# Optimization experiments

Hardware: AMD Instinct MI355X
Metric: run time of the kernel (lower is better)

## Reference

```python
import jax, jax.numpy as jnp
import numpy as np

TOPK = 4


def setup_inputs() -> dict:
    key = jax.random.key(0)
    ks = jax.random.split(key, 9)
    B, T, D = 4, 2048, 1024
    E, H = 32, 128          # routed experts, per-expert hidden
    HS = H * TOPK           # shared expert hidden = 512
    s = lambda k, shape, fan: jax.random.normal(k, shape, dtype=jnp.float32) / np.sqrt(fan)
    return {
        "x": jax.random.normal(ks[0], (B, T, D), dtype=jnp.float32),
        "router_w": s(ks[1], (E, D), D),
        "router_bias": jnp.zeros((E,), dtype=jnp.float32),
        "gate_w": s(ks[2], (E, H, D), D),
        "up_w": s(ks[3], (E, H, D), D),
        "down_w": s(ks[4], (E, D, H), H),
        "sgate_w": s(ks[5], (HS, D), D),
        "sup_w": s(ks[6], (HS, D), D),
        "sdown_w": s(ks[7], (D, HS), HS),
    }


def reference(x, router_w, router_bias, gate_w, up_w, down_w, sgate_w, sup_w, sdown_w):
    B, T, D = x.shape
    flat = x.reshape(B * T, D)                                   # [N, D]
    # Router (fp32 logits + persistent bias buffer)
    logits = flat.astype(jnp.float32) @ router_w.T + router_bias  # [N, E]
    scores = jax.nn.softmax(logits, axis=-1)
    topk_scores, topk_idx = jax.lax.top_k(scores, TOPK)          # [N, K]
    topk_scores = topk_scores / jnp.clip(
        topk_scores.sum(axis=-1, keepdims=True), 1e-12, None)
    # Dense all-expert SwiGLU (matches torch.stack over experts)
    h = jax.nn.silu(jnp.einsum("nd,ehd->neh", flat, gate_w)) \
        * jnp.einsum("nd,ehd->neh", flat, up_w)                  # [N, E, H]
    expert_out = jnp.einsum("neh,edh->ned", h, down_w)           # [N, E, D]
    # Gather top-k expert outputs, scale, combine
    sel = jnp.take_along_axis(expert_out, topk_idx[:, :, None], axis=1)  # [N, K, D]
    out = (sel * topk_scores.astype(flat.dtype)[:, :, None]).sum(axis=1)  # [N, D]
    # Always-on shared expert (SwiGLU)
    out = out + (jax.nn.silu(flat @ sgate_w.T) * (flat @ sup_w.T)) @ sdown_w.T
    return out.reshape(B, T, D)
```

## Files before the change

kernel.cpp:

```cpp
#include <hip/hip_runtime.h>
#include <hip/hip_bf16.h>
#include <math.h>

#define N_TOK 8192
#define DIM   1024
#define E_R   32
#define H_E   128
#define HS    512
#define TOPK  4
#define RKS   8
#define RKL   (DIM / RKS)
#define MAXSLOT 34816

typedef __bf16 bf16;
typedef __bf16 bf16x8 __attribute__((ext_vector_type(8)));
typedef float  floatx4 __attribute__((ext_vector_type(4)));

#define MFMA16(a,b,c) __builtin_amdgcn_mfma_f32_16x16x32_bf16(a,b,c,0,0,0)

__device__ __forceinline__ void gl_lds16(const bf16* g, bf16* l) {
    __builtin_amdgcn_global_load_lds(
        (const __attribute__((address_space(1))) void*)g,
        (__attribute__((address_space(3))) void*)l, 16, 0, 0);
}

__global__ __launch_bounds__(256)
void cvt_all(const float* __restrict__ x, const float* __restrict__ g,
             const float* __restrict__ u, const float* __restrict__ d,
             const float* __restrict__ sg, const float* __restrict__ su,
             const float* __restrict__ sd,
             bf16* __restrict__ xb, bf16* __restrict__ gb, bf16* __restrict__ ub,
             bf16* __restrict__ db, bf16* __restrict__ sgb, bf16* __restrict__ sub,
             bf16* __restrict__ sdb) {
    int b = blockIdx.x;
    const float* s; bf16* o; int lb;
    if      (b < 4096)  { s = x;  o = xb;  lb = b; }
    else if (b < 6144)  { s = g;  o = gb;  lb = b - 4096; }
    else if (b < 8192)  { s = u;  o = ub;  lb = b - 6144; }
    else if (b < 10240) { s = d;  o = db;  lb = b - 8192; }
    else if (b < 10496) { s = sg; o = sgb; lb = b - 10240; }
    else if (b < 10752) { s = su; o = sub; lb = b - 10496; }
    else                { s = sd; o = sdb; lb = b - 10752; }
    size_t i = (size_t)lb * 2048 + threadIdx.x * 8;
    float4 v0 = *(const float4*)(s + i);
    float4 v1 = *(const float4*)(s + i + 4);
    bf16x8 r = {(bf16)v0.x,(bf16)v0.y,(bf16)v0.z,(bf16)v0.w,
                (bf16)v1.x,(bf16)v1.y,(bf16)v1.z,(bf16)v1.w};
    *(bf16x8*)(o + i) = r;
}

__global__ __launch_bounds__(256)
void router_gemm(const float* __restrict__ x, const float* __restrict__ rw,
                 float* __restrict__ partial) {
    __shared__ float Xs[64 * 132];
    __shared__ float Wt[128 * 32];
    int tid = threadIdx.x;
    int t0  = blockIdx.x * 64;
    int kb  = blockIdx.y * RKL;

#pragma unroll
    for (int j = 0; j < 8; ++j) {
        int flat = j * 1024 + tid * 4;
        int row = flat >> 7, col = flat & 127;
        float4 v = *(const float4*)(x + (size_t)(t0 + row) * DIM + kb + col);
        *(float4*)(&Xs[row * 132 + col]) = v;
    }
    {
        int e = tid >> 3, kq = (tid & 7) * 16;
        const float* wp = rw + (size_t)e * DIM + kb + kq;
#pragma unroll
        for (int i = 0; i < 16; i += 4) {
            float4 v = *(const float4*)(wp + i);
            Wt[(kq + i + 0) * 32 + e] = v.x;
            Wt[(kq + i + 1) * 32 + e] = v.y;
            Wt[(kq + i + 2) * 32 + e] = v.z;
            Wt[(kq + i + 3) * 32 + e] = v.w;
        }
    }
    __syncthreads();

    int eg = tid & 7, tg = tid >> 3;
    float acc[2][4] = {{0.f}};
#pragma unroll 4
    for (int k = 0; k < RKL; k += 4) {
        float4 xa0 = *(const float4*)(&Xs[(tg * 2 + 0) * 132 + k]);
        float4 xa1 = *(const float4*)(&Xs[(tg * 2 + 1) * 132 + k]);
#pragma unroll
        for (int kk = 0; kk < 4; ++kk) {
            float4 w = *(const float4*)(&Wt[(k + kk) * 32 + eg * 4]);
            float x0 = (&xa0.x)[kk], x1 = (&xa1.x)[kk];
            acc[0][0] += x0 * w.x; acc[0][1] += x0 * w.y;
            acc[0][2] += x0 * w.z; acc[0][3] += x0 * w.w;
            acc[1][0] += x1 * w.x; acc[1][1] += x1 * w.y;
            acc[1][2] += x1 * w.z; acc[1][3] += x1 * w.w;
        }
    }
#pragma unroll
    for (int t = 0; t < 2; ++t) {
        floatx4 v = { acc[t][0], acc[t][1], acc[t][2], acc[t][3] };
        *(floatx4*)(&partial[((size_t)blockIdx.y * N_TOK + t0 + tg * 2 + t) * 32 + eg * 4]) = v;
    }
}

__global__ __launch_bounds__(256)
void router_fin(const float* __restrict__ partial, const float* __restrict__ rb,
                int* __restrict__ counts, int* __restrict__ tlist,
                float* __restrict__ slist, int* __restrict__ tok2slot) {
    __shared__ int lcnt[E_R];
    __shared__ int gbase[E_R];
    int tid = threadIdx.x;
    int n = blockIdx.x * 256 + tid;
    if (tid < E_R) lcnt[tid] = 0;
    __syncthreads();

    float lg[E_R];
#pragma unroll
    for (int e4 = 0; e4 < E_R; e4 += 4) {
        floatx4 s = {0.f, 0.f, 0.f, 0.f};
#pragma unroll
        for (int ks = 0; ks < RKS; ++ks)
            s += *(const floatx4*)(&partial[((size_t)ks * N_TOK + n) * 32 + e4]);
        lg[e4 + 0] = s[0] + rb[e4 + 0];
        lg[e4 + 1] = s[1] + rb[e4 + 1];
        lg[e4 + 2] = s[2] + rb[e4 + 2];
        lg[e4 + 3] = s[3] + rb[e4 + 3];
    }
    float mx = -1e30f;
#pragma unroll
    for (int e = 0; e < E_R; ++e) mx = fmaxf(mx, lg[e]);
    float se = 0.f;
#pragma unroll
    for (int e = 0; e < E_R; ++e) { float v = __expf(lg[e] - mx); lg[e] = v; se += v; }
    float inv = 1.f / se;

    unsigned usedMask = 0;
    int idx[TOPK]; float pv[TOPK]; int lpos[TOPK]; float psum = 0.f;
    for (int k = 0; k < TOPK; ++k) {
        float best = -1.f; int bi = 0;
        for (int e = 0; e < E_R; ++e)
            if (!((usedMask >> e) & 1) && lg[e] > best) { best = lg[e]; bi = e; }
        usedMask |= 1u << bi;
        idx[k] = bi; pv[k] = best * inv; psum += pv[k];
    }
    float norm = 1.f / fmaxf(psum, 1e-12f);
#pragma unroll
    for (int k = 0; k < TOPK; ++k)
        lpos[k] = atomicAdd(&lcnt[idx[k]], 1);
    __syncthreads();
    if (tid < E_R) gbase[tid] = atomicAdd(&counts[tid], lcnt[tid]);
    __syncthreads();
#pragma unroll
    for (int k = 0; k < TOPK; ++k) {
        int e = idx[k];
        int pos = gbase[e] + lpos[k];
        tlist[(size_t)e * N_TOK + pos] = n;
        slist[(size_t)e * N_TOK + pos] = pv[k] * norm;
        tok2slot[(size_t)n * 4 + k] = (e << 16) | pos;
    }
}

__global__ void wq_build(const int* __restrict__ counts, int* __restrict__ items,
                         int* __restrict__ nitems, int* __restrict__ expbase) {
    if (threadIdx.x == 0) {
        int n = 0, base = 0;
        for (int e = 0; e < E_R; ++e) {
            int c = counts[e];
            expbase[e] = base;
            int nt = (c + 63) >> 6;
            for (int t = 0; t < nt; ++t)
                items[n++] = (e << 24) | (t << 16) | (base + t * 64);
            base += nt * 64;
        }
        *nitems = n;
    }
}

__global__ __launch_bounds__(256, 4)
void phase1(const bf16* __restrict__ xb, const bf16* __restrict__ wg,
            const bf16* __restrict__ wu, const bf16* __restrict__ sg,
            const bf16* __restrict__ su, const int* __restrict__ counts,
            const int* __restrict__ tlist, const int* __restrict__ items,
            const int* __restrict__ nitems,
            bf16* __restrict__ Hg, bf16* __restrict__ Hs) {
    __shared__ __align__(16) bf16 As[2 * 64 * 32];
    __shared__ __align__(16) bf16 Bs[2 * 256 * 32];

    int b = blockIdx.x;
    const bf16 *gptr, *uptr;
    bf16* hout; int hstride;
    int e, lbase, cnt = 0;
    if (b < 512) {
        int c = b >> 7, t = b & 127;
        gptr = sg + (size_t)c * H_E * DIM;
        uptr = su + (size_t)c * H_E * DIM;
        hout = Hs + (size_t)t * 64 * HS + c * H_E;
        hstride = HS;
        lbase = t * 64;
        e = -1;
    } else {
        int rbk = b - 512;
        if (rbk >= *nitems) return;
        int it = items[rbk];
        e = it >> 24; int t = (it >> 16) & 0xff; int rowbase = it & 0xffff;
        gptr = wg + (size_t)e * H_E * DIM;
        uptr = wu + (size_t)e * H_E * DIM;
        hout = Hg + (size_t)rowbase * H_E;
        hstride = H_E;
        cnt = counts[e];
        lbase = t * 64;
    }

    int tid = threadIdx.x;
    int r = tid >> 2;
    int chunk = (((tid & 3) ^ ((tid >> 3) & 3))) * 8;
    int tok;
    if (e < 0) tok = lbase + r;
    else { int li = lbase + r; if (li >= cnt) li = cnt - 1; tok = tlist[(size_t)e * N_TOK + li]; }
    const bf16* aSrc = xb + (size_t)tok * DIM + chunk;
    const bf16* gSrc = gptr + (size_t)r * DIM + chunk;
    const bf16* uSrc = uptr + (size_t)r * DIM + chunk;

    int w = tid >> 6, lane = tid & 63, m = lane & 15, quad = lane >> 4;
    int quadx = quad ^ ((m >> 1) & 3);

    floatx4 aG[4][2] = {{{0}}};
    floatx4 aU[4][2] = {{{0}}};

    #define P1_STAGE(buf, k0)                                                  \
        do {                                                                   \
            bf16* aD = As + (buf) * 2048 + tid * 8;                            \
            bf16* bD = Bs + (buf) * 8192 + tid * 8;                            \
            gl_lds16(aSrc + (k0), aD);                                         \
            gl_lds16(gSrc + (k0), bD);                                         \
            gl_lds16(gSrc + 64 * DIM + (k0), bD + 2048);                       \
            gl_lds16(uSrc + (k0), bD + 4096);                                  \
            gl_lds16(uSrc + 64 * DIM + (k0), bD + 6144);                       \
        } while (0)

    P1_STAGE(0, 0);
    __syncthreads();

    int cur = 0;
    for (int k0 = 0; k0 < DIM; k0 += 32) {
        if (k0 + 32 < DIM) P1_STAGE(cur ^ 1, k0 + 32);
        const bf16* Ab = As + cur * 2048;
        const bf16* Bb = Bs + cur * 8192;
        bf16x8 a[4], bg[2], bu[2];
#pragma unroll
        for (int mg = 0; mg < 4; ++mg)
            a[mg] = *(const bf16x8*)(Ab + (mg * 16 + m) * 32 + quadx * 8);
#pragma unroll
        for (int j = 0; j < 2; ++j) {
            bg[j] = *(const bf16x8*)(Bb + (w * 32 + j * 16 + m) * 32 + quadx * 8);
            bu[j] = *(const bf16x8*)(Bb + (128 + w * 32 + j * 16 + m) * 32 + quadx * 8);
        }
#pragma unroll
        for (int j = 0; j < 2; ++j)
#pragma unroll
            for (int mg = 0; mg < 4; ++mg) {
                aG[mg][j] = MFMA16(a[mg], bg[j], aG[mg][j]);
                aU[mg][j] = MFMA16(a[mg], bu[j], aU[mg][j]);
            }
        __syncthreads();
        cur ^= 1;
    }
    #undef P1_STAGE

#pragma unroll
    for (int mg = 0; mg < 4; ++mg)
#pragma unroll
        for (int j = 0; j < 2; ++j)
#pragma unroll
            for (int r4 = 0; r4 < 4; ++r4) {
                float gv = aG[mg][j][r4], uv = aU[mg][j][r4];
                float h = gv / (1.f + __expf(-gv)) * uv;
                hout[(size_t)(mg * 16 + quad * 4 + r4) * hstride + w * 32 + j * 16 + m] = (bf16)h;
            }
}

__global__ __launch_bounds__(256, 4)
void phase2(const bf16* __restrict__ Hg, const bf16* __restrict__ wd,
            const int* __restrict__ counts, const float* __restrict__ slist,
            const int* __restrict__ items, const int* __restrict__ nitems,
            bf16* __restrict__ Od) {
    __shared__ __align__(16) bf16 As[2 * 64 * 32];
    __shared__ __align__(16) bf16 Bs[2 * 256 * 32];
    __shared__ float ssc[64];

    int rbk = blockIdx.x;
    if (rbk >= *nitems) return;
    int it = items[rbk];
    int e = it >> 24, t = (it >> 16) & 0xff, rowbase = it & 0xffff;
    int n0 = blockIdx.y * 256;
    int cnt = counts[e];

    int tid = threadIdx.x;
    if (tid < 64) {
        int li = t * 64 + tid;
        ssc[tid] = (li < cnt) ? slist[(size_t)e * N_TOK + li] : 0.f;
    }

    int r = tid >> 2;
    int chunk = (((tid & 3) ^ ((tid >> 3) & 3))) * 8;
    const bf16* aSrc = Hg + (size_t)(rowbase + r) * H_E + chunk;
    const bf16* bSrc = wd + (size_t)e * DIM * H_E + (size_t)(n0 + r) * H_E + chunk;

    int w = tid >> 6, lane = tid & 63, m = lane & 15, quad = lane >> 4;
    int quadx = quad ^ ((m >> 1) & 3);
    floatx4 acc[4][4] = {{{0}}};

    #define P2_STAGE(buf, k0)                                                  \
        do {                                                                   \
            bf16* aD = As + (buf) * 2048 + tid * 8;                            \
            bf16* bD = Bs + (buf) * 8192 + tid * 8;                            \
            gl_lds16(aSrc + (k0), aD);                                         \
            _Pragma("unroll")                                                  \
            for (int p = 0; p < 4; ++p)                                        \
                gl_lds16(bSrc + (size_t)p * 64 * H_E + (k0), bD + p * 2048);   \
        } while (0)

    P2_STAGE(0, 0);
    __syncthreads();

    int cur = 0;
    for (int k0 = 0; k0 < H_E; k0 += 32) {
        if (k0 + 32 < H_E) P2_STAGE(cur ^ 1, k0 + 32);
        const bf16* Ab = As + cur * 2048;
        const bf16* Bb = Bs + cur * 8192;
        bf16x8 a[4], bb[4];
#pragma unroll
        for (int mg = 0; mg < 4; ++mg)
            a[mg] = *(const bf16x8*)(Ab + (mg * 16 + m) * 32 + quadx * 8);
#pragma unroll
        for (int ng = 0; ng < 4; ++ng)
            bb[ng] = *(const bf16x8*)(Bb + (w * 64 + ng * 16 + m) * 32 + quadx * 8);
#pragma unroll
        for (int ng = 0; ng < 4; ++ng)
#pragma unroll
            for (int mg = 0; mg < 4; ++mg)
                acc[mg][ng] = MFMA16(a[mg], bb[ng], acc[mg][ng]);
        __syncthreads();
        cur ^= 1;
    }
    #undef P2_STAGE

#pragma unroll
    for (int mg = 0; mg < 4; ++mg)
#pragma unroll
        for (int r4 = 0; r4 < 4; ++r4) {
            int row = mg * 16 + quad * 4 + r4;
            float sc = ssc[row];
            bf16* op = Od + (size_t)(rowbase + row) * DIM + n0 + w * 64 + m;
#pragma unroll
            for (int ng = 0; ng < 4; ++ng)
                op[ng * 16] = (bf16)(acc[mg][ng][r4] * sc);
        }
}

__global__ __launch_bounds__(256, 4)
void shared_down(const bf16* __restrict__ Hs, const bf16* __restrict__ sd,
                 const bf16* __restrict__ Od, const int* __restrict__ tok2slot,
                 const int* __restrict__ expbase, float* __restrict__ out) {
    __shared__ __align__(16) bf16 As[2 * 64 * 32];
    __shared__ __align__(16) bf16 Bs[2 * 256 * 32];
    __shared__ int srow[64][4];

    int t0 = blockIdx.x * 64;
    int n0 = blockIdx.y * 256;
    int tid = threadIdx.x;

    if (tid < 64) {
        const int* t2s = tok2slot + (size_t)(t0 + tid) * 4;
#pragma unroll
        for (int k = 0; k < 4; ++k) {
            int v = t2s[k];
            srow[tid][k] = expbase[v >> 16] + (v & 0xffff);
        }
    }

    int r = tid >> 2;
    int chunk = (((tid & 3) ^ ((tid >> 3) & 3))) * 8;
    const bf16* aSrc = Hs + (size_t)(t0 + r) * HS + chunk;
    const bf16* bSrc = sd + (size_t)(n0 + r) * HS + chunk;

    int w = tid >> 6, lane = tid & 63, m = lane & 15, quad = lane >> 4;
    int quadx = quad ^ ((m >> 1) & 3);
    floatx4 acc[4][4] = {{{0}}};

    #define SD_STAGE(buf, k0)                                                  \
        do {                                                                   \
            bf16* aD = As + (buf) * 2048 + tid * 8;                            \
            bf16* bD = Bs + (buf) * 8192 + tid * 8;                            \
            gl_lds16(aSrc + (k0), aD);                                         \
            _Pragma("unroll")                                                  \
            for (int p = 0; p < 4; ++p)                                        \
                gl_lds16(bSrc + (size_t)p * 64 * HS + (k0), bD + p * 2048);    \
        } while (0)

    SD_STAGE(0, 0);
    __syncthreads();

    int cur = 0;
    for (int tt = 0; tt < 16; ++tt) {
        if (tt < 15) SD_STAGE(cur ^ 1, (tt + 1) * 32);
        const bf16* Ab = As + cur * 2048;
        const bf16* Bb = Bs + cur * 8192;
        bf16x8 a[4], bb[4];
#pragma unroll
        for (int mg = 0; mg < 4; ++mg)
            a[mg] = *(const bf16x8*)(Ab + (mg * 16 + m) * 32 + quadx * 8);
#pragma unroll
        for (int ng = 0; ng < 4; ++ng)
            bb[ng] = *(const bf16x8*)(Bb + (w * 64 + ng * 16 + m) * 32 + quadx * 8);
#pragma unroll
        for (int ng = 0; ng < 4; ++ng)
#pragma unroll
            for (int mg = 0; mg < 4; ++mg)
                acc[mg][ng] = MFMA16(a[mg], bb[ng], acc[mg][ng]);
        __syncthreads();
        cur ^= 1;
    }
    #undef SD_STAGE

#pragma unroll
    for (int mg = 0; mg < 4; ++mg)
#pragma unroll
        for (int r4 = 0; r4 < 4; ++r4) {
            int rl = mg * 16 + quad * 4 + r4;
            size_t r0 = (size_t)srow[rl][0] * DIM;
            size_t r1 = (size_t)srow[rl][1] * DIM;
            size_t r2 = (size_t)srow[rl][2] * DIM;
            size_t r3 = (size_t)srow[rl][3] * DIM;
            float* op = out + (size_t)(t0 + rl) * DIM + n0 + w * 64 + m;
#pragma unroll
            for (int ng = 0; ng < 4; ++ng) {
                int col = n0 + w * 64 + ng * 16 + m;
                float v = acc[mg][ng][r4]
                        + (float)Od[r0 + col] + (float)Od[r1 + col]
                        + (float)Od[r2 + col] + (float)Od[r3 + col];
                op[ng * 16] = v;
            }
        }
}

extern "C" void kernel_launch(void* const* d_in, const int* in_sizes, int n_in,
                              void* d_out, int out_size, void* d_ws, size_t ws_size,
                              hipStream_t stream) {
    (void)in_sizes; (void)n_in; (void)out_size; (void)ws_size;
    const float* x   = (const float*)d_in[0];
    const float* rw  = (const float*)d_in[1];
    const float* rb  = (const float*)d_in[2];
    const float* gw  = (const float*)d_in[3];
    const float* uw  = (const float*)d_in[4];
    const float* dw  = (const float*)d_in[5];
    const float* sgw = (const float*)d_in[6];
    const float* suw = (const float*)d_in[7];
    const float* sdw = (const float*)d_in[8];
    float* out = (float*)d_out;

    char* ws = (char*)d_ws;
    size_t o = 0;
    bf16* xb  = (bf16*)(ws + o); o += (size_t)N_TOK * DIM * 2;
    bf16* wgb = (bf16*)(ws + o); o += (size_t)E_R * H_E * DIM * 2;
    bf16* wub = (bf16*)(ws + o); o += (size_t)E_R * H_E * DIM * 2;
    bf16* wdb = (bf16*)(ws + o); o += (size_t)E_R * DIM * H_E * 2;
    bf16* sgb = (bf16*)(ws + o); o += (size_t)HS * DIM * 2;
    bf16* sub = (bf16*)(ws + o); o += (size_t)HS * DIM * 2;
    bf16* sdb = (bf16*)(ws + o); o += (size_t)DIM * HS * 2;
    bf16* Hg  = (bf16*)(ws + o); o += (size_t)MAXSLOT * H_E * 2;
    bf16* Hs  = (bf16*)(ws + o); o += (size_t)N_TOK * HS * 2;
    bf16* Od  = (bf16*)(ws + o); o += (size_t)MAXSLOT * DIM * 2;
    float* partial = (float*)(ws + o); o += (size_t)RKS * N_TOK * 32 * 4;
    int*   counts = (int*)(ws + o);   o += 256;
    int*   tlist  = (int*)(ws + o);   o += (size_t)E_R * N_TOK * 4;
    float* slist  = (float*)(ws + o); o += (size_t)E_R * N_TOK * 4;
    int*   tok2slot = (int*)(ws + o); o += (size_t)N_TOK * 4 * 4;
    int*   items  = (int*)(ws + o);   o += 4096;
    int*   nitems = (int*)(ws + o);   o += 64;
    int*   expbase = (int*)(ws + o);  o += 256;

    hipMemsetAsync(counts, 0, E_R * sizeof(int), stream);

    router_gemm<<<dim3(N_TOK / 64, RKS), 256, 0, stream>>>(x, rw, partial);
    router_fin<<<N_TOK / 256, 256, 0, stream>>>(partial, rb, counts, tlist, slist,
                                                tok2slot);
    cvt_all<<<11008, 256, 0, stream>>>(x, gw, uw, dw, sgw, suw, sdw,
                                       xb, wgb, wub, wdb, sgb, sub, sdb);
    wq_build<<<1, 64, 0, stream>>>(counts, items, nitems, expbase);
    phase1<<<1056, 256, 0, stream>>>(xb, wgb, wub, sgb, sub, counts, tlist,
                                     items, nitems, Hg, Hs);
    phase2<<<dim3(544, 4), 256, 0, stream>>>(Hg, wdb, counts, slist,
                                             items, nitems, Od);
    shared_down<<<dim3(N_TOK / 64, 4), 256, 0, stream>>>(Hs, sdb, Od, tok2slot,
                                                         expbase, out);
}
```

Baseline: 306.5 us.

## Scatter routed expert outputs into output via atomics, drop Od buffer

Phase2 now scales each routed-expert down-projection row and atomically adds it straight into the fp32 output at the token's row, using the token list. Shared_down runs first and writes the shared-expert result directly. This removes the bf16 Od intermediate (write plus four gathered reads per output element) and the tok2slot/expbase bookkeeping. In exchange phase2 issues 4 float atomics per output element, contended across the top-k experts, and summation order becomes nondeterministic.

Measured after the change: 511.2 us. 66.8% more time.

```diff
diff --git a/kernel.cpp b/kernel.cpp
--- a/kernel.cpp
+++ b/kernel.cpp
@@ -105,7 +105,7 @@
 __global__ __launch_bounds__(256)
 void router_fin(const float* __restrict__ partial, const float* __restrict__ rb,
                 int* __restrict__ counts, int* __restrict__ tlist,
-                float* __restrict__ slist, int* __restrict__ tok2slot) {
+                float* __restrict__ slist) {
     __shared__ int lcnt[E_R];
     __shared__ int gbase[E_R];
     int tid = threadIdx.x;
@@ -155,17 +155,15 @@
         int pos = gbase[e] + lpos[k];
         tlist[(size_t)e * N_TOK + pos] = n;
         slist[(size_t)e * N_TOK + pos] = pv[k] * norm;
-        tok2slot[(size_t)n * 4 + k] = (e << 16) | pos;
     }
 }
 
 __global__ void wq_build(const int* __restrict__ counts, int* __restrict__ items,
-                         int* __restrict__ nitems, int* __restrict__ expbase) {
+                         int* __restrict__ nitems) {
     if (threadIdx.x == 0) {
         int n = 0, base = 0;
         for (int e = 0; e < E_R; ++e) {
             int c = counts[e];
-            expbase[e] = base;
             int nt = (c + 63) >> 6;
             for (int t = 0; t < nt; ++t)
                 items[n++] = (e << 24) | (t << 16) | (base + t * 64);
@@ -281,11 +279,12 @@
 __global__ __launch_bounds__(256, 4)
 void phase2(const bf16* __restrict__ Hg, const bf16* __restrict__ wd,
             const int* __restrict__ counts, const float* __restrict__ slist,
-            const int* __restrict__ items, const int* __restrict__ nitems,
-            bf16* __restrict__ Od) {
+            const int* __restrict__ tlist, const int* __restrict__ items,
+            const int* __restrict__ nitems, float* __restrict__ out) {
     __shared__ __align__(16) bf16 As[2 * 64 * 32];
     __shared__ __align__(16) bf16 Bs[2 * 256 * 32];
     __shared__ float ssc[64];
+    __shared__ int   stok[64];
 
     int rbk = blockIdx.x;
     if (rbk >= *nitems) return;
@@ -297,7 +296,9 @@
     int tid = threadIdx.x;
     if (tid < 64) {
         int li = t * 64 + tid;
-        ssc[tid] = (li < cnt) ? slist[(size_t)e * N_TOK + li] : 0.f;
+        bool ok = (li < cnt);
+        ssc[tid]  = ok ? slist[(size_t)e * N_TOK + li] : 0.f;
+        stok[tid] = ok ? tlist[(size_t)e * N_TOK + li] : 0;
     }
 
     int r = tid >> 2;
@@ -350,33 +351,22 @@
         for (int r4 = 0; r4 < 4; ++r4) {
             int row = mg * 16 + quad * 4 + r4;
             float sc = ssc[row];
-            bf16* op = Od + (size_t)(rowbase + row) * DIM + n0 + w * 64 + m;
+            float* op = out + (size_t)stok[row] * DIM + n0 + w * 64 + m;
 #pragma unroll
             for (int ng = 0; ng < 4; ++ng)
-                op[ng * 16] = (bf16)(acc[mg][ng][r4] * sc);
+                atomicAdd(op + ng * 16, acc[mg][ng][r4] * sc);
         }
 }
 
 __global__ __launch_bounds__(256, 4)
 void shared_down(const bf16* __restrict__ Hs, const bf16* __restrict__ sd,
-                 const bf16* __restrict__ Od, const int* __restrict__ tok2slot,
-                 const int* __restrict__ expbase, float* __restrict__ out) {
+                 float* __restrict__ out) {
     __shared__ __align__(16) bf16 As[2 * 64 * 32];
     __shared__ __align__(16) bf16 Bs[2 * 256 * 32];
-    __shared__ int srow[64][4];
 
     int t0 = blockIdx.x * 64;
     int n0 = blockIdx.y * 256;
     int tid = threadIdx.x;
-
-    if (tid < 64) {
-        const int* t2s = tok2slot + (size_t)(t0 + tid) * 4;
-#pragma unroll
-        for (int k = 0; k < 4; ++k) {
-            int v = t2s[k];
-            srow[tid][k] = expbase[v >> 16] + (v & 0xffff);
-        }
-    }
 
     int r = tid >> 2;
     int chunk = (((tid & 3) ^ ((tid >> 3) & 3))) * 8;
@@ -427,19 +417,10 @@
 #pragma unroll
         for (int r4 = 0; r4 < 4; ++r4) {
             int rl = mg * 16 + quad * 4 + r4;
-            size_t r0 = (size_t)srow[rl][0] * DIM;
-            size_t r1 = (size_t)srow[rl][1] * DIM;
-            size_t r2 = (size_t)srow[rl][2] * DIM;
-            size_t r3 = (size_t)srow[rl][3] * DIM;
             float* op = out + (size_t)(t0 + rl) * DIM + n0 + w * 64 + m;
 #pragma unroll
-            for (int ng = 0; ng < 4; ++ng) {
-                int col = n0 + w * 64 + ng * 16 + m;
-                float v = acc[mg][ng][r4]
-                        + (float)Od[r0 + col] + (float)Od[r1 + col]
-                        + (float)Od[r2 + col] + (float)Od[r3 + col];
-                op[ng * 16] = v;
-            }
+            for (int ng = 0; ng < 4; ++ng)
+                op[ng * 16] = acc[mg][ng][r4];
         }
 }
 
@@ -469,28 +450,23 @@
     bf16* sdb = (bf16*)(ws + o); o += (size_t)DIM * HS * 2;
     bf16* Hg  = (bf16*)(ws + o); o += (size_t)MAXSLOT * H_E * 2;
     bf16* Hs  = (bf16*)(ws + o); o += (size_t)N_TOK * HS * 2;
-    bf16* Od  = (bf16*)(ws + o); o += (size_t)MAXSLOT * DIM * 2;
     float* partial = (float*)(ws + o); o += (size_t)RKS * N_TOK * 32 * 4;
     int*   counts = (int*)(ws + o);   o += 256;
     int*   tlist  = (int*)(ws + o);   o += (size_t)E_R * N_TOK * 4;
     float* slist  = (float*)(ws + o); o += (size_t)E_R * N_TOK * 4;
-    int*   tok2slot = (int*)(ws + o); o += (size_t)N_TOK * 4 * 4;
     int*   items  = (int*)(ws + o);   o += 4096;
     int*   nitems = (int*)(ws + o);   o += 64;
-    int*   expbase = (int*)(ws + o);  o += 256;
 
     hipMemsetAsync(counts, 0, E_R * sizeof(int), stream);
 
     router_gemm<<<dim3(N_TOK / 64, RKS), 256, 0, stream>>>(x, rw, partial);
-    router_fin<<<N_TOK / 256, 256, 0, stream>>>(partial, rb, counts, tlist, slist,
-                                                tok2slot);
+    router_fin<<<N_TOK / 256, 256, 0, stream>>>(partial, rb, counts, tlist, slist);
     cvt_all<<<11008, 256, 0, stream>>>(x, gw, uw, dw, sgw, suw, sdw,
                                        xb, wgb, wub, wdb, sgb, sub, sdb);
-    wq_build<<<1, 64, 0, stream>>>(counts, items, nitems, expbase);
+    wq_build<<<1, 64, 0, stream>>>(counts, items, nitems);
     phase1<<<1056, 256, 0, stream>>>(xb, wgb, wub, sgb, sub, counts, tlist,
                                      items, nitems, Hg, Hs);
-    phase2<<<dim3(544, 4), 256, 0, stream>>>(Hg, wdb, counts, slist,
-                                             items, nitems, Od);
-    shared_down<<<dim3(N_TOK / 64, 4), 256, 0, stream>>>(Hs, sdb, Od, tok2slot,
-                                                         expbase, out);
-}
+    shared_down<<<dim3(N_TOK / 64, 4), 256, 0, stream>>>(Hs, sdb, out);
+    phase2<<<dim3(544, 4), 256, 0, stream>>>(Hg, wdb, counts, slist, tlist,
+                                             items, nitems, out);
+}
```

## Double phase1 token tile to 128 rows to halve weight reloads

Applied to the files above, without the earlier changes.

Phase1 now processes 128 tokens per block instead of 64, so each block loads gate/up weight tiles once for twice as many rows, doubling arithmetic per weight byte. The work queue builder emits separate item lists: 128-row items for phase1 and 64-row items for phase2, with per-expert slot padding rounded to 128, which increases MAXSLOT. The cost is twice the accumulator registers (launch bounds lowered to 2 blocks per CU), fewer phase1 blocks, and more padded rows for small experts.

Measured after the change: 318.3 us. 1.04x slower.

```diff
diff --git a/kernel.cpp b/kernel.cpp
--- a/kernel.cpp
+++ b/kernel.cpp
@@ -10,7 +10,7 @@
 #define TOPK  4
 #define RKS   8
 #define RKL   (DIM / RKS)
-#define MAXSLOT 34816
+#define MAXSLOT 36864
 
 typedef __bf16 bf16;
 typedef __bf16 bf16x8 __attribute__((ext_vector_type(8)));
@@ -159,46 +159,50 @@
     }
 }
 
-__global__ void wq_build(const int* __restrict__ counts, int* __restrict__ items,
-                         int* __restrict__ nitems, int* __restrict__ expbase) {
+__global__ void wq_build(const int* __restrict__ counts, int* __restrict__ items1,
+                         int* __restrict__ nitems1, int* __restrict__ items2,
+                         int* __restrict__ nitems2, int* __restrict__ expbase) {
     if (threadIdx.x == 0) {
-        int n = 0, base = 0;
+        int n1 = 0, n2 = 0, base = 0;
         for (int e = 0; e < E_R; ++e) {
             int c = counts[e];
             expbase[e] = base;
-            int nt = (c + 63) >> 6;
+            int nt = (c + 127) >> 7;
             for (int t = 0; t < nt; ++t)
-                items[n++] = (e << 24) | (t << 16) | (base + t * 64);
-            base += nt * 64;
-        }
-        *nitems = n;
-    }
-}
-
-__global__ __launch_bounds__(256, 4)
+                items1[n1++] = (e << 24) | (t << 16) | (base + t * 128);
+            for (int t = 0; t < nt * 2; ++t)
+                items2[n2++] = (e << 24) | (t << 16) | (base + t * 64);
+            base += nt * 128;
+        }
+        *nitems1 = n1;
+        *nitems2 = n2;
+    }
+}
+
+__global__ __launch_bounds__(256, 2)
 void phase1(const bf16* __restrict__ xb, const bf16* __restrict__ wg,
             const bf16* __restrict__ wu, const bf16* __restrict__ sg,
             const bf16* __restrict__ su, const int* __restrict__ counts,
             const int* __restrict__ tlist, const int* __restrict__ items,
             const int* __restrict__ nitems,
             bf16* __restrict__ Hg, bf16* __restrict__ Hs) {
-    __shared__ __align__(16) bf16 As[2 * 64 * 32];
+    __shared__ __align__(16) bf16 As[2 * 128 * 32];
     __shared__ __align__(16) bf16 Bs[2 * 256 * 32];
 
     int b = blockIdx.x;
     const bf16 *gptr, *uptr;
     bf16* hout; int hstride;
     int e, lbase, cnt = 0;
-    if (b < 512) {
-        int c = b >> 7, t = b & 127;
+    if (b < 256) {
+        int c = b >> 6, t = b & 63;
         gptr = sg + (size_t)c * H_E * DIM;
         uptr = su + (size_t)c * H_E * DIM;
-        hout = Hs + (size_t)t * 64 * HS + c * H_E;
+        hout = Hs + (size_t)t * 128 * HS + c * H_E;
         hstride = HS;
-        lbase = t * 64;
+        lbase = t * 128;
         e = -1;
     } else {
-        int rbk = b - 512;
+        int rbk = b - 256;
         if (rbk >= *nitems) return;
         int it = items[rbk];
         e = it >> 24; int t = (it >> 16) & 0xff; int rowbase = it & 0xffff;
@@ -207,33 +211,40 @@
         hout = Hg + (size_t)rowbase * H_E;
         hstride = H_E;
         cnt = counts[e];
-        lbase = t * 64;
+        lbase = t * 128;
     }
 
     int tid = threadIdx.x;
     int r = tid >> 2;
     int chunk = (((tid & 3) ^ ((tid >> 3) & 3))) * 8;
-    int tok;
-    if (e < 0) tok = lbase + r;
-    else { int li = lbase + r; if (li >= cnt) li = cnt - 1; tok = tlist[(size_t)e * N_TOK + li]; }
-    const bf16* aSrc = xb + (size_t)tok * DIM + chunk;
-    const bf16* gSrc = gptr + (size_t)r * DIM + chunk;
-    const bf16* uSrc = uptr + (size_t)r * DIM + chunk;
+    int tokA, tokB;
+    if (e < 0) { tokA = lbase + r; tokB = lbase + r + 64; }
+    else {
+        int liA = lbase + r;      if (liA >= cnt) liA = cnt - 1;
+        int liB = lbase + r + 64; if (liB >= cnt) liB = cnt - 1;
+        tokA = tlist[(size_t)e * N_TOK + liA];
+        tokB = tlist[(size_t)e * N_TOK + liB];
+    }
+    const bf16* aSrc0 = xb + (size_t)tokA * DIM + chunk;
+    const bf16* aSrc1 = xb + (size_t)tokB * DIM + chunk;
+    const bf16* gSrc  = gptr + (size_t)r * DIM + chunk;
+    const bf16* uSrc  = uptr + (size_t)r * DIM + chunk;
 
     int w = tid >> 6, lane = tid & 63, m = lane & 15, quad = lane >> 4;
-    int quadx = quad ^ ((m >> 1) & 3);
-
-    floatx4 aG[4][2] = {{{0}}};
-    floatx4 aU[4][2] = {{{0}}};
+    int cx = (quad ^ ((m >> 1) & 3)) * 8;
+
+    floatx4 aG[8][2] = {{{0}}};
+    floatx4 aU[8][2] = {{{0}}};
 
     #define P1_STAGE(buf, k0)                                                  \
         do {                                                                   \
-            bf16* aD = As + (buf) * 2048 + tid * 8;                            \
+            bf16* aD = As + (buf) * 4096 + tid * 8;                            \
             bf16* bD = Bs + (buf) * 8192 + tid * 8;                            \
-            gl_lds16(aSrc + (k0), aD);                                         \
-            gl_lds16(gSrc + (k0), bD);                                         \
+            gl_lds16(aSrc0 + (k0), aD);                                        \
+            gl_lds16(aSrc1 + (k0), aD + 2048);                                 \
+            gl_lds16(gSrc + (k0),            bD);                              \
             gl_lds16(gSrc + 64 * DIM + (k0), bD + 2048);                       \
-            gl_lds16(uSrc + (k0), bD + 4096);                                  \
+            gl_lds16(uSrc + (k0),            bD + 4096);                       \
             gl_lds16(uSrc + 64 * DIM + (k0), bD + 6144);                       \
         } while (0)
 
@@ -243,31 +254,29 @@
     int cur = 0;
     for (int k0 = 0; k0 < DIM; k0 += 32) {
         if (k0 + 32 < DIM) P1_STAGE(cur ^ 1, k0 + 32);
-        const bf16* Ab = As + cur * 2048;
+        const bf16* Ab = As + cur * 4096;
         const bf16* Bb = Bs + cur * 8192;
-        bf16x8 a[4], bg[2], bu[2];
-#pragma unroll
-        for (int mg = 0; mg < 4; ++mg)
-            a[mg] = *(const bf16x8*)(Ab + (mg * 16 + m) * 32 + quadx * 8);
+        bf16x8 bg[2], bu[2];
 #pragma unroll
         for (int j = 0; j < 2; ++j) {
-            bg[j] = *(const bf16x8*)(Bb + (w * 32 + j * 16 + m) * 32 + quadx * 8);
-            bu[j] = *(const bf16x8*)(Bb + (128 + w * 32 + j * 16 + m) * 32 + quadx * 8);
-        }
-#pragma unroll
-        for (int j = 0; j < 2; ++j)
-#pragma unroll
-            for (int mg = 0; mg < 4; ++mg) {
-                aG[mg][j] = MFMA16(a[mg], bg[j], aG[mg][j]);
-                aU[mg][j] = MFMA16(a[mg], bu[j], aU[mg][j]);
-            }
+            bg[j] = *(const bf16x8*)(Bb + (w * 32 + j * 16 + m) * 32 + cx);
+            bu[j] = *(const bf16x8*)(Bb + (128 + w * 32 + j * 16 + m) * 32 + cx);
+        }
+#pragma unroll
+        for (int mg = 0; mg < 8; ++mg) {
+            bf16x8 a = *(const bf16x8*)(Ab + (mg * 16 + m) * 32 + cx);
+            aG[mg][0] = MFMA16(a, bg[0], aG[mg][0]);
+            aG[mg][1] = MFMA16(a, bg[1], aG[mg][1]);
+            aU[mg][0] = MFMA16(a, bu[0], aU[mg][0]);
+            aU[mg][1] = MFMA16(a, bu[1], aU[mg][1]);
+        }
         __syncthreads();
         cur ^= 1;
     }
     #undef P1_STAGE
 
 #pragma unroll
-    for (int mg = 0; mg < 4; ++mg)
+    for (int mg = 0; mg < 8; ++mg)
 #pragma unroll
         for (int j = 0; j < 2; ++j)
 #pragma unroll
@@ -475,8 +484,10 @@
     int*   tlist  = (int*)(ws + o);   o += (size_t)E_R * N_TOK * 4;
     float* slist  = (float*)(ws + o); o += (size_t)E_R * N_TOK * 4;
     int*   tok2slot = (int*)(ws + o); o += (size_t)N_TOK * 4 * 4;
-    int*   items  = (int*)(ws + o);   o += 4096;
-    int*   nitems = (int*)(ws + o);   o += 64;
+    int*   items1 = (int*)(ws + o);   o += 4096;
+    int*   items2 = (int*)(ws + o);   o += 4096;
+    int*   nitems1 = (int*)(ws + o);  o += 64;
+    int*   nitems2 = (int*)(ws + o);  o += 64;
     int*   expbase = (int*)(ws + o);  o += 256;
 
     hipMemsetAsync(counts, 0, E_R * sizeof(int), stream);
@@ -486,11 +497,12 @@
                                                 tok2slot);
     cvt_all<<<11008, 256, 0, stream>>>(x, gw, uw, dw, sgw, suw, sdw,
                                        xb, wgb, wub, wdb, sgb, sub, sdb);
-    wq_build<<<1, 64, 0, stream>>>(counts, items, nitems, expbase);
-    phase1<<<1056, 256, 0, stream>>>(xb, wgb, wub, sgb, sub, counts, tlist,
-                                     items, nitems, Hg, Hs);
-    phase2<<<dim3(544, 4), 256, 0, stream>>>(Hg, wdb, counts, slist,
-                                             items, nitems, Od);
+    wq_build<<<1, 64, 0, stream>>>(counts, items1, nitems1, items2, nitems2,
+                                   expbase);
+    phase1<<<544, 256, 0, stream>>>(xb, wgb, wub, sgb, sub, counts, tlist,
+                                    items1, nitems1, Hg, Hs);
+    phase2<<<dim3(576, 4), 256, 0, stream>>>(Hg, wdb, counts, slist,
+                                             items2, nitems2, Od);
     shared_down<<<dim3(N_TOK / 64, 4), 256, 0, stream>>>(Hs, sdb, Od, tok2slot,
                                                          expbase, out);
 }
```

## Double phase1 K-tile to 64 and add XCD-aware block swizzling

Applied to the files above, without the earlier changes.

Phase1 now stages 64-wide K slices per iteration, with a new 8-way XOR LDS swizzle and two A-row loads per thread. This halves the number of barriers and loop iterations, at the cost of doubling LDS use and lowering the occupancy hint from 4 to 2 blocks per CU. All three GEMM kernels also remap block indices so that consecutive logical blocks land on the same XCD, to improve L2 reuse of shared expert weights. The swizzle relies on hardcoded grid sizes (1056, 544, 128) that must match the launch configuration.

Measured after the change: 292.4 us. 4.6% less time.

```diff
diff --git a/kernel.cpp b/kernel.cpp
--- a/kernel.cpp
+++ b/kernel.cpp
@@ -22,6 +22,12 @@
     __builtin_amdgcn_global_load_lds(
         (const __attribute__((address_space(1))) void*)g,
         (__attribute__((address_space(3))) void*)l, 16, 0, 0);
+}
+
+__device__ __forceinline__ int xcd_swz(int b, int n) {
+    int q = n >> 3, r = n & 7;
+    int xcd = b & 7, idx = b >> 3;
+    return (xcd < r ? xcd * (q + 1) : r * (q + 1) + (xcd - r) * q) + idx;
 }
 
 __global__ __launch_bounds__(256)
@@ -175,17 +181,17 @@
     }
 }
 
-__global__ __launch_bounds__(256, 4)
+__global__ __launch_bounds__(256, 2)
 void phase1(const bf16* __restrict__ xb, const bf16* __restrict__ wg,
             const bf16* __restrict__ wu, const bf16* __restrict__ sg,
             const bf16* __restrict__ su, const int* __restrict__ counts,
             const int* __restrict__ tlist, const int* __restrict__ items,
             const int* __restrict__ nitems,
             bf16* __restrict__ Hg, bf16* __restrict__ Hs) {
-    __shared__ __align__(16) bf16 As[2 * 64 * 32];
-    __shared__ __align__(16) bf16 Bs[2 * 256 * 32];
-
-    int b = blockIdx.x;
+    __shared__ __align__(16) bf16 As[2 * 64 * 64];
+    __shared__ __align__(16) bf16 Bs[2 * 256 * 64];
+
+    int b = xcd_swz(blockIdx.x, 1056);
     const bf16 *gptr, *uptr;
     bf16* hout; int hstride;
     int e, lbase, cnt = 0;
@@ -211,56 +217,71 @@
     }
 
     int tid = threadIdx.x;
-    int r = tid >> 2;
-    int chunk = (((tid & 3) ^ ((tid >> 3) & 3))) * 8;
-    int tok;
-    if (e < 0) tok = lbase + r;
-    else { int li = lbase + r; if (li >= cnt) li = cnt - 1; tok = tlist[(size_t)e * N_TOK + li]; }
-    const bf16* aSrc = xb + (size_t)tok * DIM + chunk;
-    const bf16* gSrc = gptr + (size_t)r * DIM + chunk;
-    const bf16* uSrc = uptr + (size_t)r * DIM + chunk;
+    int rs = tid >> 3;
+    int cOff = ((tid & 7) ^ (rs & 7)) * 8;
+    int tokA, tokB;
+    if (e < 0) { tokA = lbase + rs; tokB = lbase + rs + 32; }
+    else {
+        int liA = lbase + rs;      if (liA >= cnt) liA = cnt - 1;
+        int liB = lbase + rs + 32; if (liB >= cnt) liB = cnt - 1;
+        tokA = tlist[(size_t)e * N_TOK + liA];
+        tokB = tlist[(size_t)e * N_TOK + liB];
+    }
+    const bf16* aSrc0 = xb + (size_t)tokA * DIM + cOff;
+    const bf16* aSrc1 = xb + (size_t)tokB * DIM + cOff;
+    const bf16* gSrc  = gptr + (size_t)rs * DIM + cOff;
+    const bf16* uSrc  = uptr + (size_t)rs * DIM + cOff;
 
     int w = tid >> 6, lane = tid & 63, m = lane & 15, quad = lane >> 4;
-    int quadx = quad ^ ((m >> 1) & 3);
+    int mx7 = m & 7;
 
     floatx4 aG[4][2] = {{{0}}};
     floatx4 aU[4][2] = {{{0}}};
 
     #define P1_STAGE(buf, k0)                                                  \
         do {                                                                   \
-            bf16* aD = As + (buf) * 2048 + tid * 8;                            \
-            bf16* bD = Bs + (buf) * 8192 + tid * 8;                            \
-            gl_lds16(aSrc + (k0), aD);                                         \
-            gl_lds16(gSrc + (k0), bD);                                         \
-            gl_lds16(gSrc + 64 * DIM + (k0), bD + 2048);                       \
-            gl_lds16(uSrc + (k0), bD + 4096);                                  \
-            gl_lds16(uSrc + 64 * DIM + (k0), bD + 6144);                       \
+            bf16* aD = As + (buf) * 4096 + tid * 8;                            \
+            bf16* bD = Bs + (buf) * 16384 + tid * 8;                           \
+            gl_lds16(aSrc0 + (k0), aD);                                        \
+            gl_lds16(aSrc1 + (k0), aD + 2048);                                 \
+            gl_lds16(gSrc + (k0),            bD);                              \
+            gl_lds16(gSrc + 32 * DIM + (k0), bD + 2048);                       \
+            gl_lds16(gSrc + 64 * DIM + (k0), bD + 4096);                       \
+            gl_lds16(gSrc + 96 * DIM + (k0), bD + 6144);                       \
+            gl_lds16(uSrc + (k0),            bD + 8192);                       \
+            gl_lds16(uSrc + 32 * DIM + (k0), bD + 10240);                      \
+            gl_lds16(uSrc + 64 * DIM + (k0), bD + 12288);                      \
+            gl_lds16(uSrc + 96 * DIM + (k0), bD + 14336);                      \
         } while (0)
 
     P1_STAGE(0, 0);
     __syncthreads();
 
     int cur = 0;
-    for (int k0 = 0; k0 < DIM; k0 += 32) {
-        if (k0 + 32 < DIM) P1_STAGE(cur ^ 1, k0 + 32);
-        const bf16* Ab = As + cur * 2048;
-        const bf16* Bb = Bs + cur * 8192;
-        bf16x8 a[4], bg[2], bu[2];
-#pragma unroll
-        for (int mg = 0; mg < 4; ++mg)
-            a[mg] = *(const bf16x8*)(Ab + (mg * 16 + m) * 32 + quadx * 8);
-#pragma unroll
-        for (int j = 0; j < 2; ++j) {
-            bg[j] = *(const bf16x8*)(Bb + (w * 32 + j * 16 + m) * 32 + quadx * 8);
-            bu[j] = *(const bf16x8*)(Bb + (128 + w * 32 + j * 16 + m) * 32 + quadx * 8);
-        }
-#pragma unroll
-        for (int j = 0; j < 2; ++j)
-#pragma unroll
-            for (int mg = 0; mg < 4; ++mg) {
-                aG[mg][j] = MFMA16(a[mg], bg[j], aG[mg][j]);
-                aU[mg][j] = MFMA16(a[mg], bu[j], aU[mg][j]);
+    for (int k0 = 0; k0 < DIM; k0 += 64) {
+        if (k0 + 64 < DIM) P1_STAGE(cur ^ 1, k0 + 64);
+        const bf16* Ab = As + cur * 4096;
+        const bf16* Bb = Bs + cur * 16384;
+#pragma unroll
+        for (int kh = 0; kh < 2; ++kh) {
+            int cx = ((kh * 4 + quad) ^ mx7) * 8;
+            bf16x8 a[4], bg[2], bu[2];
+#pragma unroll
+            for (int mg = 0; mg < 4; ++mg)
+                a[mg] = *(const bf16x8*)(Ab + (mg * 16 + m) * 64 + cx);
+#pragma unroll
+            for (int j = 0; j < 2; ++j) {
+                bg[j] = *(const bf16x8*)(Bb + (w * 32 + j * 16 + m) * 64 + cx);
+                bu[j] = *(const bf16x8*)(Bb + (128 + w * 32 + j * 16 + m) * 64 + cx);
             }
+#pragma unroll
+            for (int j = 0; j < 2; ++j)
+#pragma unroll
+                for (int mg = 0; mg < 4; ++mg) {
+                    aG[mg][j] = MFMA16(a[mg], bg[j], aG[mg][j]);
+                    aU[mg][j] = MFMA16(a[mg], bu[j], aU[mg][j]);
+                }
+        }
         __syncthreads();
         cur ^= 1;
     }
@@ -287,7 +308,7 @@
     __shared__ __align__(16) bf16 Bs[2 * 256 * 32];
     __shared__ float ssc[64];
 
-    int rbk = blockIdx.x;
+    int rbk = xcd_swz(blockIdx.x, 544);
     if (rbk >= *nitems) return;
     int it = items[rbk];
     int e = it >> 24, t = (it >> 16) & 0xff, rowbase = it & 0xffff;
@@ -365,7 +386,7 @@
     __shared__ __align__(16) bf16 Bs[2 * 256 * 32];
     __shared__ int srow[64][4];
 
-    int t0 = blockIdx.x * 64;
+    int t0 = xcd_swz(blockIdx.x, 128) * 64;
     int n0 = blockIdx.y * 256;
     int tid = threadIdx.x;
 
```
